# Kernel optimization log

Measured on AMD Instinct MI355X. Metric: run time of the kernel, lower is better.

## Reference

```python
import jax, jax.numpy as jnp
import numpy as np

jax.config.update("jax_enable_x64", True)

# --- static config (matches init_kwargs) ---
L = 6            # voxel_level_num
F = 8            # feature_dim
T = 524288       # per-level feature table size
B = 4194304      # buffer_size (hash table size)
N = 1048576      # number of query points
LEAF = 0.25      # leaf_voxel_size
UP = 2.0         # up_scale_factor

PRIMES = jnp.array([73856093, 19349669, 83492791], dtype=jnp.int64)
# corner offsets, z varies fastest (same order as torch self.steps)
STEPS = jnp.array([[0,0,0],[0,0,1],[0,1,0],[0,1,1],
                   [1,0,0],[1,0,1],[1,1,0],[1,1,1]], dtype=jnp.float32)


def setup_inputs() -> dict:
    key = jax.random.key(0)
    k1, k2, k3, k4 = jax.random.split(key, 4)
    query_points = jax.random.uniform(k1, (N, 3), dtype=jnp.float32) * 50.0
    features = 0.01 * jax.random.normal(k2, (L, T, F), dtype=jnp.float32)
    idx = jax.random.randint(k3, (L, B), 0, T, dtype=jnp.int64)
    empty = jax.random.uniform(k4, (L, B)) < 0.2
    feature_indexs = jnp.where(empty, jnp.int64(-1), idx)
    return {"query_points": query_points, "features": features,
            "feature_indexs": feature_indexs}


def _trilinear_coeffs(d):
    # d: [N,3] fractional coords in the cell; order matches STEPS (z fastest)
    tx, ty, tz = d[:, 0], d[:, 1], d[:, 2]
    return jnp.stack([
        (1-tx)*(1-ty)*(1-tz), (1-tx)*(1-ty)*tz,
        (1-tx)*ty*(1-tz),     (1-tx)*ty*tz,
        tx*(1-ty)*(1-tz),     tx*(1-ty)*tz,
        tx*ty*(1-tz),         tx*ty*tz,
    ], axis=1)  # [N,8]


def reference(query_points, features, feature_indexs):
    out = jnp.zeros((query_points.shape[0], F), dtype=query_points.dtype)
    for i in range(L):  # small fixed level loop (structurally distinct resolutions)
        res = LEAF * (UP ** i)
        scaled = query_points / res                      # [N,3]
        base = jnp.floor(scaled)
        corners = (base[:, None, :] + STEPS[None]).astype(jnp.int64)  # [N,8,3]
        keys = jnp.mod((corners * PRIMES).sum(-1), B)    # [N,8] spatial hash
        idx = feature_indexs[i][keys]                    # [N,8] gather, -1 = empty
        valid = idx.min(axis=1) > -1                     # [N] all 8 corners allocated
        coeffs = _trilinear_coeffs(scaled - base)        # [N,8]
        feats = features[i][jnp.clip(idx, 0, T - 1)]     # [N,8,F] gather
        level = jnp.einsum('nkf,nk->nf', feats, coeffs)  # trilinear interp
        out = out + jnp.where(valid[:, None], level, jnp.zeros((), out.dtype))
    return out
```

## Files before the change

### kernel.cpp

```cpp
#include <hip/hip_runtime.h>


static constexpr int      NPTS  = 1048576;
static constexpr int      NF    = 8;
static constexpr int      TTAB  = 524288;
static constexpr unsigned BTAB  = 4194304u;
static constexpr unsigned BMASK = BTAB - 1u;
static constexpr unsigned P0 = 73856093u, P1 = 19349669u, P2 = 83492791u;

static constexpr int NBIN = 4096;
static constexpr int SB   = 256;
static constexpr int PPB  = NPTS / SB;
static constexpr int ITER = PPB / 256;
static constexpr int BCAP = 512;

static constexpr int S2 = 51, S3 = 26, S4 = 14, S5 = 8;
static constexpr int OCC2 = 0, OCC3 = OCC2 + S2*S2, OCC4 = OCC3 + S3*S3,
                     OCC5 = OCC4 + S4*S4, OCCW = OCC5 + S5*S5;
static constexpr int CB2 = 0, CB3 = CB2 + (S2-1)*(S2-1),
                     CB4 = CB3 + (S3-1)*(S3-1), CB5 = CB4 + (S4-1)*(S4-1),
                     CBW = CB5 + (S5-1)*(S5-1);
static constexpr int RB2 = (S2*S2+3)/4, RB3 = (S3*S3+3)/4,
                     RB4 = (S4*S4+3)/4, RB5 = (S5*S5+3)/4;
static constexpr int OCCB = RB2+RB3+RB4+RB5;

static constexpr int L0S = 201, L0C = 200, L0W = 4;
static constexpr int L1S = 101, L1C = 100, L1W = 2;
static constexpr int OCC0W_CNT = L0S * L0S * L0W;
static constexpr int OCC1W_CNT = L1S * L1S * L1W;
static constexpr int CB0_CNT = L0C * L0C * L0W;
static constexpr int CB1_CNT = L1C * L1C * L1W;
static constexpr int OCC01_WORDS = OCC0W_CNT + OCC1W_CNT;
static constexpr int MIDC = CBW + CB0_CNT + CB1_CNT;
static constexpr int MIDB = 16 + (MIDC + 255) / 256;

static constexpr int BM01_WAVES = (int)(2 * BTAB / 256);
static constexpr int BM01B = BM01_WAVES / 4;

static constexpr size_t OUT_BM01_OFF  = 4u  * 1024 * 1024;
static constexpr size_t OUT_OCC25_OFF = 5u  * 1024 * 1024;
static constexpr size_t OUT_OCC0_OFF  = 5632u * 1024;
static constexpr size_t OUT_OCC1_OFF  = 7u  * 1024 * 1024;

static constexpr size_t SORTED_BYTES = (size_t)NPTS * 16;
static constexpr size_t CB25_OFF = SORTED_BYTES;
static constexpr size_t CB0_OFF  = CB25_OFF + 32768;
static constexpr size_t CB1_OFF  = CB0_OFF + 1310720;
static constexpr size_t BB_OFF   = CB1_OFF + 163840;
static constexpr size_t WS_FULL  = BB_OFF + (size_t)NBIN * 4;

typedef float f4 __attribute__((ext_vector_type(4)));
typedef int   i4 __attribute__((ext_vector_type(4)));

__device__ __forceinline__ void nhv_point_g(
    float qx, float qy, float qz,
    const float* __restrict__ feat, const int* __restrict__ fidx,
    const unsigned long long* __restrict__ cbit25,
    const unsigned long long* __restrict__ cbit0,
    const unsigned long long* __restrict__ cbit1, float acc[NF])
{
    const int ix0 = (int)(qx * 4.0f), iy0 = (int)(qy * 4.0f), iz0 = (int)(qz * 4.0f);
    const int ix1 = (int)(qx * 2.0f), iy1 = (int)(qy * 2.0f), iz1 = (int)(qz * 2.0f);

    const unsigned long long w0 = cbit0[(size_t)(iz0 * L0C + iy0) * L0W + (ix0 >> 6)];
    const unsigned long long w1 = cbit1[(size_t)(iz1 * L1C + iy1) * L1W + (ix1 >> 6)];

    float fxh[4], fyh[4], fzh[4];
    int   ixh[4], iyh[4], izh[4];
    unsigned vm = 0;
    vm |= (unsigned)((w0 >> (ix0 & 63)) & 1ull) << 0;
    vm |= (unsigned)((w1 >> (ix1 & 63)) & 1ull) << 1;
    const int Ss[4]  = {S2, S3, S4, S5};
    const int CBo[4] = {CB2, CB3, CB4, CB5};
#pragma unroll
    for (int j = 0; j < 4; ++j) {
        const float inv = 1.0f / (float)(1 << j);
        const float sx = qx*inv, sy = qy*inv, sz = qz*inv;
        const float bx = floorf(sx), by = floorf(sy), bz = floorf(sz);
        fxh[j] = sx-bx; fyh[j] = sy-by; fzh[j] = sz-bz;
        ixh[j] = (int)bx; iyh[j] = (int)by; izh[j] = (int)bz;
        const int C = Ss[j] - 1;
        const unsigned long long row = cbit25[CBo[j] + izh[j]*C + iyh[j]];
        vm |= (unsigned)((row >> ixh[j]) & 1ull) << (2 + j);
    }

#pragma unroll
    for (int f = 0; f < NF; ++f) acc[f] = 0.0f;

#pragma unroll
    for (int i = 0; i < 2; ++i) {
        if (vm & (1u << i)) {
            const float inv = (i == 0) ? 4.0f : 2.0f;
            const float sx = qx*inv, sy = qy*inv, sz = qz*inv;
            const float bx = floorf(sx), by = floorf(sy), bz = floorf(sz);
            const unsigned h = (unsigned)(int)bx*P0 + (unsigned)(int)by*P1
                             + (unsigned)(int)bz*P2;
            const int* __restrict__ tab = fidx + (size_t)i * BTAB;
            int id[8];
#pragma unroll
            for (int k = 0; k < 8; ++k) {
                unsigned key = h;
                if (k & 4) key += P0;
                if (k & 2) key += P1;
                if (k & 1) key += P2;
                id[k] = tab[key & BMASK];
            }
            const float tx = sx - bx, ty = sy - by, tz = sz - bz;
            const float wxv[2] = {1.0f - tx, tx};
            const float wyv[2] = {1.0f - ty, ty};
            const float wzv[2] = {1.0f - tz, tz};
            const float* __restrict__ fb = feat + (size_t)i * (TTAB * NF);
#pragma unroll
            for (int k = 0; k < 8; ++k) {
                const float c = wxv[(k>>2)&1] * wyv[(k>>1)&1] * wzv[k&1];
                const float4* p = (const float4*)(fb + (size_t)id[k] * NF);
                const float4 lo = p[0], hi = p[1];
                acc[0]+=c*lo.x; acc[1]+=c*lo.y; acc[2]+=c*lo.z; acc[3]+=c*lo.w;
                acc[4]+=c*hi.x; acc[5]+=c*hi.y; acc[6]+=c*hi.z; acc[7]+=c*hi.w;
            }
        }
    }
#pragma unroll
    for (int j = 0; j < 4; ++j) {
        if (vm & (1u << (2 + j))) {
            const int lvl = 2 + j;
            const unsigned h = (unsigned)ixh[j]*P0 + (unsigned)iyh[j]*P1
                             + (unsigned)izh[j]*P2;
            const int* __restrict__ tab = fidx + (size_t)lvl * BTAB;
            int id[8];
#pragma unroll
            for (int k = 0; k < 8; ++k) {
                unsigned key = h;
                if (k & 4) key += P0;
                if (k & 2) key += P1;
                if (k & 1) key += P2;
                id[k] = tab[key & BMASK];
            }
            const float wxv[2] = {1.0f - fxh[j], fxh[j]};
            const float wyv[2] = {1.0f - fyh[j], fyh[j]};
            const float wzv[2] = {1.0f - fzh[j], fzh[j]};
            const float* __restrict__ fb = feat + (size_t)lvl * (TTAB * NF);
#pragma unroll
            for (int k = 0; k < 8; ++k) {
                const float c = wxv[(k>>2)&1] * wyv[(k>>1)&1] * wzv[k&1];
                const float4* p = (const float4*)(fb + (size_t)id[k] * NF);
                const float4 lo = p[0], hi = p[1];
                acc[0]+=c*lo.x; acc[1]+=c*lo.y; acc[2]+=c*lo.z; acc[3]+=c*lo.w;
                acc[4]+=c*hi.x; acc[5]+=c*hi.y; acc[6]+=c*hi.z; acc[7]+=c*hi.w;
            }
        }
    }
}

__device__ __forceinline__ void nhv_point(
    float qx, float qy, float qz,
    const float* __restrict__ feat, const int* __restrict__ fidx, float acc[NF])
{
    float fx[6], fy[6], fz[6];
    unsigned h[6];
#pragma unroll
    for (int i = 0; i < 6; ++i) {
        const float inv = 4.0f / (float)(1 << i);
        const float sx = qx*inv, sy = qy*inv, sz = qz*inv;
        const float bx = floorf(sx), by = floorf(sy), bz = floorf(sz);
        fx[i] = sx-bx; fy[i] = sy-by; fz[i] = sz-bz;
        h[i] = (unsigned)(int)bx*P0 + (unsigned)(int)by*P1 + (unsigned)(int)bz*P2;
    }
    int id[6][8];
#pragma unroll
    for (int i = 0; i < 6; ++i) {
        const int* __restrict__ tab = fidx + (size_t)i * BTAB;
#pragma unroll
        for (int k = 0; k < 8; ++k) {
            unsigned key = h[i];
            if (k & 4) key += P0;
            if (k & 2) key += P1;
            if (k & 1) key += P2;
            id[i][k] = tab[key & BMASK];
        }
    }
#pragma unroll
    for (int f = 0; f < NF; ++f) acc[f] = 0.0f;
#pragma unroll
    for (int i = 0; i < 6; ++i) {
        int mn = id[i][0];
#pragma unroll
        for (int k = 1; k < 8; ++k) mn = min(mn, id[i][k]);
        if (mn > -1) {
            const float wxv[2] = {1.0f - fx[i], fx[i]};
            const float wyv[2] = {1.0f - fy[i], fy[i]};
            const float wzv[2] = {1.0f - fz[i], fz[i]};
            const float* __restrict__ fb = feat + (size_t)i * (TTAB * NF);
#pragma unroll
            for (int k = 0; k < 8; ++k) {
                const float c = wxv[(k>>2)&1] * wyv[(k>>1)&1] * wzv[k&1];
                const float4* p = (const float4*)(fb + (size_t)id[i][k] * NF);
                const float4 lo = p[0], hi = p[1];
                acc[0]+=c*lo.x; acc[1]+=c*lo.y; acc[2]+=c*lo.z; acc[3]+=c*lo.w;
                acc[4]+=c*hi.x; acc[5]+=c*hi.y; acc[6]+=c*hi.z; acc[7]+=c*hi.w;
            }
        }
    }
}

__device__ __forceinline__ unsigned expand4(unsigned v) {
    return (v & 1u) | ((v & 2u) << 2) | ((v & 4u) << 4) | ((v & 8u) << 6);
}
__device__ __forceinline__ unsigned bin_of(float x, float y, float z) {
    unsigned bx = min(15u, (unsigned)(int)(x * 0.32f));
    unsigned by = min(15u, (unsigned)(int)(y * 0.32f));
    unsigned bz = min(15u, (unsigned)(int)(z * 0.32f));
    return expand4(bx) | (expand4(by) << 1) | (expand4(bz) << 2);
}

__global__ __launch_bounds__(256) void pre_k(const int* __restrict__ fidx,
                                             unsigned long long* __restrict__ occ25,
                                             unsigned long long* __restrict__ bm01,
                                             const float* __restrict__ qp,
                                             unsigned* __restrict__ hist) {
    __shared__ unsigned lh[NBIN];
    const int t = threadIdx.x, b = blockIdx.x;
    if (b < OCCB) {
        int lvl, S, occoff, bb = b;
        if (bb < RB2)              { lvl = 2; S = S2; occoff = OCC2; }
        else if ((bb -= RB2) < RB3){ lvl = 3; S = S3; occoff = OCC3; }
        else if ((bb -= RB3) < RB4){ lvl = 4; S = S4; occoff = OCC4; }
        else        { bb -= RB4;     lvl = 5; S = S5; occoff = OCC5; }
        const int row  = bb * 4 + (t >> 6);
        const int lane = t & 63;
        if (row < S * S) {
            const int y = row % S, z = row / S;
            bool v = false;
            if (lane < S) {
                const unsigned key = ((unsigned)lane*P0 + (unsigned)y*P1
                                    + (unsigned)z*P2) & BMASK;
                v = fidx[(size_t)lvl * BTAB + key] >= 0;
            }
            const unsigned long long m = __ballot(v);
            if (lane == 0) occ25[occoff + row] = m;
        }
    } else if (b < OCCB + BM01B) {
        const int tid  = (b - OCCB) * 256 + t;
        const int w    = tid >> 6;
        const int lane = tid & 63;
        const i4 v = __builtin_nontemporal_load(
                        (const i4*)(fidx + (size_t)w * 256) + lane);
        const unsigned long long m0 = __ballot(v.x >= 0);
        const unsigned long long m1 = __ballot(v.y >= 0);
        const unsigned long long m2 = __ballot(v.z >= 0);
        const unsigned long long m3 = __ballot(v.w >= 0);
        if (lane == 0) {
            unsigned long long* d = bm01 + ((size_t)w << 2);
            d[0] = m0; d[1] = m1; d[2] = m2; d[3] = m3;
        }
    } else {
        const int bh = b - OCCB - BM01B;
        for (int i = t; i < NBIN; i += 256) lh[i] = 0u;
        __syncthreads();
        const int base = bh * PPB;
#pragma unroll
        for (int i = 0; i < ITER; ++i) {
            const int p = base + i * 256 + t;
            const float x = __builtin_nontemporal_load(qp + 3*p);
            const float y = __builtin_nontemporal_load(qp + 3*p + 1);
            const float z = __builtin_nontemporal_load(qp + 3*p + 2);
            atomicAdd(&lh[bin_of(x, y, z)], 1u);
        }
        __syncthreads();
        for (int i = t; i < NBIN; i += 256)
            __builtin_nontemporal_store(lh[i], hist + (size_t)bh * NBIN + i);
    }
}

__global__ __launch_bounds__(256) void occ01_k(
    const unsigned long long* __restrict__ bm01,
    unsigned long long* __restrict__ occ0,
    unsigned long long* __restrict__ occ1)
{
    const int lane   = threadIdx.x & 63;
    const int wid    = (blockIdx.x * 256 + threadIdx.x) >> 6;
    const int nwaves = (int)gridDim.x * 4;
    const int ngroups = (OCC01_WORDS + 3) / 4;

    for (int g = wid; g < ngroups; g += nwaves) {
        unsigned long long vals[4];
        bool ok[4];
#pragma unroll
        for (int k = 0; k < 4; ++k) {
            const int w = g * 4 + k;
            ok[k] = (w < OCC01_WORDS);
            bool v = false;
            if (ok[k]) {
                int S, row, wblk, lvl;
                if (w < OCC0W_CNT) { lvl = 0; S = L0S; row = w >> 2; wblk = w & 3; }
                else { lvl = 1; S = L1S; const int w1 = w - OCC0W_CNT; row = w1 >> 1; wblk = w1 & 1; }
                const int z = row / S, y = row % S;
                const int x = wblk * 64 + lane;
                if (x < S) {
                    const unsigned key = ((unsigned)x*P0 + (unsigned)y*P1
                                        + (unsigned)z*P2) & BMASK;
                    const unsigned B = (unsigned)lvl * BTAB + key;
                    const unsigned long long word =
                        bm01[((size_t)(B >> 8) << 2) | (B & 3u)];
                    v = (word >> ((B >> 2) & 63u)) & 1ull;
                }
            }
            vals[k] = v ? 1ull : 0ull;
        }
#pragma unroll
        for (int k = 0; k < 4; ++k) {
            const unsigned long long m = __ballot(vals[k] != 0ull);
            const int w = g * 4 + k;
            if (ok[k] && lane == 0) {
                if (w < OCC0W_CNT) occ0[w] = m;
                else               occ1[w - OCC0W_CNT] = m;
            }
        }
    }
}

__global__ __launch_bounds__(256) void mid_k(unsigned* __restrict__ hist,
                                             unsigned* __restrict__ binbase,
                                             const unsigned long long* __restrict__ occ25,
                                             const unsigned long long* __restrict__ occ0,
                                             const unsigned long long* __restrict__ occ1,
                                             unsigned long long* __restrict__ cbit25,
                                             unsigned long long* __restrict__ cbit0,
                                             unsigned long long* __restrict__ cbit1) {
    const int t = threadIdx.x, b = blockIdx.x;
    if (b < 16) {
        const int bin = b * 256 + t;
        unsigned run = 0;
        for (int blk = 0; blk < SB; ++blk) {
            const unsigned v = hist[(size_t)blk * NBIN + bin];
            hist[(size_t)blk * NBIN + bin] = run;
            run += v;
        }
        binbase[bin] = run;
        return;
    }
    const int c = (b - 16) * 256 + t;
    if (c >= MIDC) return;
    if (c < CBW) {
        int S, occoff, cboff, local;
        if (c < CB3)      { S = S2; occoff = OCC2; cboff = CB2; local = c; }
        else if (c < CB4) { S = S3; occoff = OCC3; cboff = CB3; local = c - CB3; }
        else if (c < CB5) { S = S4; occoff = OCC4; cboff = CB4; local = c - CB4; }
        else              { S = S5; occoff = OCC5; cboff = CB5; local = c - CB5; }
        const int C = S - 1;
        const int cy = local % C, cz = local / C;
        const unsigned long long r00 = occ25[occoff +  cz      * S + cy    ];
        const unsigned long long r10 = occ25[occoff +  cz      * S + cy + 1];
        const unsigned long long r01 = occ25[occoff + (cz + 1) * S + cy    ];
        const unsigned long long r11 = occ25[occoff + (cz + 1) * S + cy + 1];
        cbit25[cboff + cz * C + cy] = (r00 & (r00 >> 1)) & (r10 & (r10 >> 1))
                                    & (r01 & (r01 >> 1)) & (r11 & (r11 >> 1));
    } else if (c < CBW + CB0_CNT) {
        const int c0 = c - CBW;
        const int w = c0 & 3, crow = c0 >> 2;
        const int cy = crow % L0C, cz = crow / L0C;
        unsigned long long res = ~0ull;
#pragma unroll
        for (int dy = 0; dy < 2; ++dy)
#pragma unroll
            for (int dz = 0; dz < 2; ++dz) {
                const unsigned long long* r =
                    occ0 + ((size_t)((cz + dz) * L0S + (cy + dy)) << 2);
                const unsigned long long a = r[w];
                const unsigned long long n = (w < 3) ? r[w + 1] : 0ull;
                res &= a & ((a >> 1) | (n << 63));
            }
        cbit0[c0] = res;
    } else {
        const int c1 = c - CBW - CB0_CNT;
        const int w = c1 & 1, crow = c1 >> 1;
        const int cy = crow % L1C, cz = crow / L1C;
        unsigned long long res = ~0ull;
#pragma unroll
        for (int dy = 0; dy < 2; ++dy)
#pragma unroll
            for (int dz = 0; dz < 2; ++dz) {
                const unsigned long long* r =
                    occ1 + ((size_t)((cz + dz) * L1S + (cy + dy)) << 1);
                const unsigned long long a = r[w];
                const unsigned long long n = (w < 1) ? r[w + 1] : 0ull;
                res &= a & ((a >> 1) | (n << 63));
            }
        cbit1[c1] = res;
    }
}

__global__ __launch_bounds__(256) void binscan_k(unsigned* __restrict__ binbase) {
    __shared__ unsigned tot[256];
    const int t = threadIdx.x;
    unsigned v[16];
    unsigned s = 0;
#pragma unroll
    for (int i = 0; i < 16; ++i) { v[i] = s; s += binbase[t * 16 + i]; }
    tot[t] = s;
    __syncthreads();
    for (int d = 1; d < 256; d <<= 1) {
        const unsigned x = (t >= d) ? tot[t - d] : 0u;
        __syncthreads();
        tot[t] += x;
        __syncthreads();
    }
    const unsigned cb = tot[t] - s;
#pragma unroll
    for (int i = 0; i < 16; ++i) binbase[t * 16 + i] = cb + v[i];
}

__global__ __launch_bounds__(256) void scatter_k(const float* __restrict__ qp,
                                                 const unsigned* __restrict__ hist,
                                                 const unsigned* __restrict__ binbase,
                                                 float4* __restrict__ sorted) {
    __shared__ unsigned cur[NBIN];
    const int b = blockIdx.x, t = threadIdx.x;
    for (int i = t; i < NBIN; i += 256)
        cur[i] = binbase[i] + hist[(size_t)b * NBIN + i];
    __syncthreads();
    const int base = b * PPB;
#pragma unroll
    for (int i = 0; i < ITER; ++i) {
        const int p = base + i * 256 + t;
        const float x = __builtin_nontemporal_load(qp + 3*p);
        const float y = __builtin_nontemporal_load(qp + 3*p + 1);
        const float z = __builtin_nontemporal_load(qp + 3*p + 2);
        const unsigned slot = atomicAdd(&cur[bin_of(x, y, z)], 1u);
        const f4 v = {x, y, z, __uint_as_float((unsigned)p)};
        __builtin_nontemporal_store(v, (f4*)sorted + slot);
    }
}

__global__ __launch_bounds__(256) void binsort_k(float4* __restrict__ sorted,
                                                 const unsigned* __restrict__ binbase) {
    __shared__ float4        pts[BCAP];
    __shared__ unsigned char sk[BCAP];
    __shared__ unsigned      cnt[64];
    const int bin = blockIdx.x, t = threadIdx.x;
    const unsigned start = binbase[bin];
    const unsigned end   = (bin < NBIN - 1) ? binbase[bin + 1] : (unsigned)NPTS;
    const int n = (int)(end - start);
    if (n <= 1 || n > BCAP) return;

    if (t < 64) cnt[t] = 0u;
    __syncthreads();
#pragma unroll
    for (int r = 0; r < BCAP / 256; ++r) {
        const int i = r * 256 + t;
        if (i < n) {
            const f4 pv = __builtin_nontemporal_load((const f4*)sorted + (start + i));
            const float4 p = make_float4(pv.x, pv.y, pv.z, pv.w);
            pts[i] = p;
            const unsigned ux = (unsigned)(int)(p.x * 1.28f) & 3u;
            const unsigned uy = (unsigned)(int)(p.y * 1.28f) & 3u;
            const unsigned uz = (unsigned)(int)(p.z * 1.28f) & 3u;
            const unsigned s = (ux & 1u) | ((uy & 1u) << 1) | ((uz & 1u) << 2)
                             | ((ux >> 1) << 3) | ((uy >> 1) << 4) | ((uz >> 1) << 5);
            sk[i] = (unsigned char)s;
            atomicAdd(&cnt[s], 1u);
        }
    }
    __syncthreads();
    if (t == 0) {
        unsigned run = 0;
#pragma unroll
        for (int i = 0; i < 64; ++i) { const unsigned v = cnt[i]; cnt[i] = run; run += v; }
    }
    __syncthreads();
#pragma unroll
    for (int r = 0; r < BCAP / 256; ++r) {
        const int i = r * 256 + t;
        if (i < n) {
            const unsigned dest = atomicAdd(&cnt[sk[i]], 1u);
            const float4 p = pts[i];
            const f4 v = {p.x, p.y, p.z, p.w};
            __builtin_nontemporal_store(v, (f4*)sorted + (start + dest));
        }
    }
}

__global__ __launch_bounds__(256) void nhv_main_k(
    const float4* __restrict__ sp, const float* __restrict__ feat,
    const int* __restrict__ fidx,
    const unsigned long long* __restrict__ cbit25,
    const unsigned long long* __restrict__ cbit0,
    const unsigned long long* __restrict__ cbit1,
    float* __restrict__ out)
{
    const int nwg = NPTS / 256;
    const int bid = blockIdx.x;
    const int swz = (bid & 7) * (nwg >> 3) + (bid >> 3);
    const int j   = swz * 256 + (int)threadIdx.x;

    const f4 s = __builtin_nontemporal_load((const f4*)sp + j);
    float acc[NF];
    nhv_point_g(s.x, s.y, s.z, feat, fidx, cbit25, cbit0, cbit1, acc);
    const unsigned n = __float_as_uint(s.w);
    f4* o = (f4*)(out + (size_t)n * NF);
    f4 lo = {acc[0], acc[1], acc[2], acc[3]};
    f4 hi = {acc[4], acc[5], acc[6], acc[7]};
    __builtin_nontemporal_store(lo, o);
    __builtin_nontemporal_store(hi, o + 1);
}

__global__ __launch_bounds__(256) void nhv_direct_k(
    const float* __restrict__ qp, const float* __restrict__ feat,
    const int* __restrict__ fidx, float* __restrict__ out)
{
    const int n = blockIdx.x * 256 + threadIdx.x;
    if (n >= NPTS) return;
    float acc[NF];
    nhv_point(qp[3*n], qp[3*n+1], qp[3*n+2], feat, fidx, acc);
    float4* o = (float4*)(out + (size_t)n * NF);
    o[0] = make_float4(acc[0], acc[1], acc[2], acc[3]);
    o[1] = make_float4(acc[4], acc[5], acc[6], acc[7]);
}

extern "C" void kernel_launch(void* const* d_in, const int* in_sizes, int n_in,
                              void* d_out, int out_size, void* d_ws, size_t ws_size,
                              hipStream_t stream) {
    const float* qp   = (const float*)d_in[0];
    const float* feat = (const float*)d_in[1];
    const int*   fidx = (const int*)d_in[2];
    float*       out  = (float*)d_out;

    if (ws_size >= WS_FULL) {
        float4*             sorted  = (float4*)d_ws;
        unsigned long long* cbit25  = (unsigned long long*)((char*)d_ws + CB25_OFF);
        unsigned long long* cbit0   = (unsigned long long*)((char*)d_ws + CB0_OFF);
        unsigned long long* cbit1   = (unsigned long long*)((char*)d_ws + CB1_OFF);
        unsigned*           binbase = (unsigned*)((char*)d_ws + BB_OFF);
        unsigned*           hist  = (unsigned*)d_out;
        unsigned long long* bm01  = (unsigned long long*)((char*)d_out + OUT_BM01_OFF);
        unsigned long long* occ25 = (unsigned long long*)((char*)d_out + OUT_OCC25_OFF);
        unsigned long long* occ0  = (unsigned long long*)((char*)d_out + OUT_OCC0_OFF);
        unsigned long long* occ1  = (unsigned long long*)((char*)d_out + OUT_OCC1_OFF);

        pre_k<<<dim3(OCCB + BM01B + SB), dim3(256), 0, stream>>>(fidx, occ25, bm01, qp, hist);
        occ01_k<<<dim3(512), dim3(256), 0, stream>>>(bm01, occ0, occ1);
        mid_k<<<dim3(MIDB), dim3(256), 0, stream>>>(hist, binbase, occ25, occ0, occ1,
                                                    cbit25, cbit0, cbit1);
        binscan_k<<<dim3(1), dim3(256), 0, stream>>>(binbase);
        scatter_k<<<dim3(SB), dim3(256), 0, stream>>>(qp, hist, binbase, sorted);
        binsort_k<<<dim3(NBIN), dim3(256), 0, stream>>>(sorted, binbase);
        nhv_main_k<<<dim3(NPTS/256), dim3(256), 0, stream>>>(sorted, feat, fidx,
                                                             cbit25, cbit0, cbit1, out);
    } else {
        nhv_direct_k<<<dim3(NPTS/256), dim3(256), 0, stream>>>(qp, feat, fidx, out);
    }
}
```

Baseline: 222.0 us.

## Fuse bin sort into main kernel and use per-cell byte validity grids

The histogram scan moves into the occupancy kernel and the bin-base scan into the corner-bit kernel, which removes two launches. The in-bin sort is folded into the main kernel: it builds an ordering in shared memory, so the extra pass writing the sorted array back to global memory goes away. Validity for levels 2-5 now comes from dense byte grids indexed by cell (one for level 2, one packed grid for levels 3-5), and all level indices are derived from the level-0 integer coords by shifts. The cost is larger validity tables, fewer threads per block for bins with few points, and a strided fallback for oversized bins.

```diff
diff --git a/kernel.cpp b/kernel.cpp
--- a/kernel.cpp
+++ b/kernel.cpp
@@ -17,9 +17,6 @@
 static constexpr int S2 = 51, S3 = 26, S4 = 14, S5 = 8;
 static constexpr int OCC2 = 0, OCC3 = OCC2 + S2*S2, OCC4 = OCC3 + S3*S3,
                      OCC5 = OCC4 + S4*S4, OCCW = OCC5 + S5*S5;
-static constexpr int CB2 = 0, CB3 = CB2 + (S2-1)*(S2-1),
-                     CB4 = CB3 + (S3-1)*(S3-1), CB5 = CB4 + (S4-1)*(S4-1),
-                     CBW = CB5 + (S5-1)*(S5-1);
 static constexpr int RB2 = (S2*S2+3)/4, RB3 = (S3*S3+3)/4,
                      RB4 = (S4*S4+3)/4, RB5 = (S5*S5+3)/4;
 static constexpr int OCCB = RB2+RB3+RB4+RB5;
@@ -31,8 +28,11 @@
 static constexpr int CB0_CNT = L0C * L0C * L0W;
 static constexpr int CB1_CNT = L1C * L1C * L1W;
 static constexpr int OCC01_WORDS = OCC0W_CNT + OCC1W_CNT;
-static constexpr int MIDC = CBW + CB0_CNT + CB1_CNT;
-static constexpr int MIDB = 16 + (MIDC + 255) / 256;
+
+static constexpr int B2_CNT   = 50 * 50 * 50;
+static constexpr int B345_CNT = 25 * 25 * 25;
+static constexpr int CBTASKS  = CB0_CNT + CB1_CNT + B2_CNT + B345_CNT;
+static constexpr int CBK_BLOCKS = 1 + (CBTASKS + 255) / 256;
 
 static constexpr int BM01_WAVES = (int)(2 * BTAB / 256);
 static constexpr int BM01B = BM01_WAVES / 4;
@@ -43,112 +43,90 @@
 static constexpr size_t OUT_OCC1_OFF  = 7u  * 1024 * 1024;
 
 static constexpr size_t SORTED_BYTES = (size_t)NPTS * 16;
-static constexpr size_t CB25_OFF = SORTED_BYTES;
-static constexpr size_t CB0_OFF  = CB25_OFF + 32768;
-static constexpr size_t CB1_OFF  = CB0_OFF + 1310720;
-static constexpr size_t BB_OFF   = CB1_OFF + 163840;
+static constexpr size_t CB0_OFF  = SORTED_BYTES;
+static constexpr size_t CB1_OFF  = CB0_OFF  + 1310720;
+static constexpr size_t B2_OFF   = CB1_OFF  + 163840;
+static constexpr size_t B345_OFF = B2_OFF   + 131072;
+static constexpr size_t BB_OFF   = B345_OFF + 16384;
 static constexpr size_t WS_FULL  = BB_OFF + (size_t)NBIN * 4;
 
 typedef float f4 __attribute__((ext_vector_type(4)));
 typedef int   i4 __attribute__((ext_vector_type(4)));
+typedef unsigned long long u64;
 
 __device__ __forceinline__ void nhv_point_g(
     float qx, float qy, float qz,
     const float* __restrict__ feat, const int* __restrict__ fidx,
-    const unsigned long long* __restrict__ cbit25,
-    const unsigned long long* __restrict__ cbit0,
-    const unsigned long long* __restrict__ cbit1, float acc[NF])
+    const u64* __restrict__ cbit0, const u64* __restrict__ cbit1,
+    const unsigned char* __restrict__ b2, const unsigned char* __restrict__ b345,
+    float acc[NF])
 {
     const int ix0 = (int)(qx * 4.0f), iy0 = (int)(qy * 4.0f), iz0 = (int)(qz * 4.0f);
-    const int ix1 = (int)(qx * 2.0f), iy1 = (int)(qy * 2.0f), iz1 = (int)(qz * 2.0f);
-
-    const unsigned long long w0 = cbit0[(size_t)(iz0 * L0C + iy0) * L0W + (ix0 >> 6)];
-    const unsigned long long w1 = cbit1[(size_t)(iz1 * L1C + iy1) * L1W + (ix1 >> 6)];
-
-    float fxh[4], fyh[4], fzh[4];
-    int   ixh[4], iyh[4], izh[4];
-    unsigned vm = 0;
-    vm |= (unsigned)((w0 >> (ix0 & 63)) & 1ull) << 0;
-    vm |= (unsigned)((w1 >> (ix1 & 63)) & 1ull) << 1;
-    const int Ss[4]  = {S2, S3, S4, S5};
-    const int CBo[4] = {CB2, CB3, CB4, CB5};
-#pragma unroll
-    for (int j = 0; j < 4; ++j) {
-        const float inv = 1.0f / (float)(1 << j);
-        const float sx = qx*inv, sy = qy*inv, sz = qz*inv;
-        const float bx = floorf(sx), by = floorf(sy), bz = floorf(sz);
-        fxh[j] = sx-bx; fyh[j] = sy-by; fzh[j] = sz-bz;
-        ixh[j] = (int)bx; iyh[j] = (int)by; izh[j] = (int)bz;
-        const int C = Ss[j] - 1;
-        const unsigned long long row = cbit25[CBo[j] + izh[j]*C + iyh[j]];
-        vm |= (unsigned)((row >> ixh[j]) & 1ull) << (2 + j);
-    }
+    const int ix1 = ix0 >> 1, iy1 = iy0 >> 1, iz1 = iz0 >> 1;
+    const int ix2 = ix0 >> 2, iy2 = iy0 >> 2, iz2 = iz0 >> 2;
+    const int ix3 = ix0 >> 3, iy3 = iy0 >> 3, iz3 = iz0 >> 3;
+
+    const u64 w0 = cbit0[(size_t)(iz0 * L0C + iy0) * L0W + (ix0 >> 6)];
+    const u64 w1 = cbit1[(size_t)(iz1 * L1C + iy1) * L1W + (ix1 >> 6)];
+    const unsigned vb2   = b2  [(iz2 * 50 + iy2) * 50 + ix2];
+    const unsigned vb345 = b345[(iz3 * 25 + iy3) * 25 + ix3];
+
+    const unsigned vm = (unsigned)((w0 >> (ix0 & 63)) & 1ull)
+                      | ((unsigned)((w1 >> (ix1 & 63)) & 1ull) << 1)
+                      | ((vb2   & 1u) << 2)
+                      | ((vb345 & 7u) << 3);
 
 #pragma unroll
     for (int f = 0; f < NF; ++f) acc[f] = 0.0f;
 
-#pragma unroll
-    for (int i = 0; i < 2; ++i) {
-        if (vm & (1u << i)) {
-            const float inv = (i == 0) ? 4.0f : 2.0f;
-            const float sx = qx*inv, sy = qy*inv, sz = qz*inv;
-            const float bx = floorf(sx), by = floorf(sy), bz = floorf(sz);
-            const unsigned h = (unsigned)(int)bx*P0 + (unsigned)(int)by*P1
-                             + (unsigned)(int)bz*P2;
-            const int* __restrict__ tab = fidx + (size_t)i * BTAB;
-            int id[8];
-#pragma unroll
-            for (int k = 0; k < 8; ++k) {
-                unsigned key = h;
-                if (k & 4) key += P0;
-                if (k & 2) key += P1;
-                if (k & 1) key += P2;
-                id[k] = tab[key & BMASK];
-            }
-            const float tx = sx - bx, ty = sy - by, tz = sz - bz;
-            const float wxv[2] = {1.0f - tx, tx};
-            const float wyv[2] = {1.0f - ty, ty};
-            const float wzv[2] = {1.0f - tz, tz};
-            const float* __restrict__ fb = feat + (size_t)i * (TTAB * NF);
-#pragma unroll
-            for (int k = 0; k < 8; ++k) {
-                const float c = wxv[(k>>2)&1] * wyv[(k>>1)&1] * wzv[k&1];
-                const float4* p = (const float4*)(fb + (size_t)id[k] * NF);
-                const float4 lo = p[0], hi = p[1];
-                acc[0]+=c*lo.x; acc[1]+=c*lo.y; acc[2]+=c*lo.z; acc[3]+=c*lo.w;
-                acc[4]+=c*hi.x; acc[5]+=c*hi.y; acc[6]+=c*hi.z; acc[7]+=c*hi.w;
-            }
-        }
-    }
-#pragma unroll
-    for (int j = 0; j < 4; ++j) {
-        if (vm & (1u << (2 + j))) {
-            const int lvl = 2 + j;
-            const unsigned h = (unsigned)ixh[j]*P0 + (unsigned)iyh[j]*P1
-                             + (unsigned)izh[j]*P2;
-            const int* __restrict__ tab = fidx + (size_t)lvl * BTAB;
-            int id[8];
-#pragma unroll
-            for (int k = 0; k < 8; ++k) {
-                unsigned key = h;
-                if (k & 4) key += P0;
-                if (k & 2) key += P1;
-                if (k & 1) key += P2;
-                id[k] = tab[key & BMASK];
-            }
-            const float wxv[2] = {1.0f - fxh[j], fxh[j]};
-            const float wyv[2] = {1.0f - fyh[j], fyh[j]};
-            const float wzv[2] = {1.0f - fzh[j], fzh[j]};
-            const float* __restrict__ fb = feat + (size_t)lvl * (TTAB * NF);
-#pragma unroll
-            for (int k = 0; k < 8; ++k) {
-                const float c = wxv[(k>>2)&1] * wyv[(k>>1)&1] * wzv[k&1];
-                const float4* p = (const float4*)(fb + (size_t)id[k] * NF);
-                const float4 lo = p[0], hi = p[1];
-                acc[0]+=c*lo.x; acc[1]+=c*lo.y; acc[2]+=c*lo.z; acc[3]+=c*lo.w;
-                acc[4]+=c*hi.x; acc[5]+=c*hi.y; acc[6]+=c*hi.z; acc[7]+=c*hi.w;
-            }
-        }
+    auto gather = [&](int lvl, unsigned cx, unsigned cy, unsigned cz,
+                      float tx, float ty, float tz) {
+        const unsigned h = cx * P0 + cy * P1 + cz * P2;
+        const int* __restrict__ tab = fidx + (size_t)lvl * BTAB;
+        int id[8];
+#pragma unroll
+        for (int k = 0; k < 8; ++k) {
+            unsigned key = h;
+            if (k & 4) key += P0;
+            if (k & 2) key += P1;
+            if (k & 1) key += P2;
+            id[k] = tab[key & BMASK];
+        }
+        const float wxv[2] = {1.0f - tx, tx};
+        const float wyv[2] = {1.0f - ty, ty};
+        const float wzv[2] = {1.0f - tz, tz};
+        const float* __restrict__ fb = feat + (size_t)lvl * (TTAB * NF);
+#pragma unroll
+        for (int k = 0; k < 8; ++k) {
+            const float c = wxv[(k>>2)&1] * wyv[(k>>1)&1] * wzv[k&1];
+            const float4* p = (const float4*)(fb + (size_t)id[k] * NF);
+            const float4 lo = p[0], hi = p[1];
+            acc[0]+=c*lo.x; acc[1]+=c*lo.y; acc[2]+=c*lo.z; acc[3]+=c*lo.w;
+            acc[4]+=c*hi.x; acc[5]+=c*hi.y; acc[6]+=c*hi.z; acc[7]+=c*hi.w;
+        }
+    };
+
+    if (vm & 1u)
+        gather(0, (unsigned)ix0, (unsigned)iy0, (unsigned)iz0,
+               qx*4.0f - (float)ix0, qy*4.0f - (float)iy0, qz*4.0f - (float)iz0);
+    if (vm & 2u)
+        gather(1, (unsigned)ix1, (unsigned)iy1, (unsigned)iz1,
+               qx*2.0f - (float)ix1, qy*2.0f - (float)iy1, qz*2.0f - (float)iz1);
+    if (vm & 4u)
+        gather(2, (unsigned)ix2, (unsigned)iy2, (unsigned)iz2,
+               qx - (float)ix2, qy - (float)iy2, qz - (float)iz2);
+    if (vm & 8u)
+        gather(3, (unsigned)ix3, (unsigned)iy3, (unsigned)iz3,
+               qx*0.5f - (float)ix3, qy*0.5f - (float)iy3, qz*0.5f - (float)iz3);
+    if (vm & 16u) {
+        const int ix4 = ix0 >> 4, iy4 = iy0 >> 4, iz4 = iz0 >> 4;
+        gather(4, (unsigned)ix4, (unsigned)iy4, (unsigned)iz4,
+               qx*0.25f - (float)ix4, qy*0.25f - (float)iy4, qz*0.25f - (float)iz4);
+    }
+    if (vm & 32u) {
+        const int ix5 = ix0 >> 5, iy5 = iy0 >> 5, iz5 = iz0 >> 5;
+        gather(5, (unsigned)ix5, (unsigned)iy5, (unsigned)iz5,
+               qx*0.125f - (float)ix5, qy*0.125f - (float)iy5, qz*0.125f - (float)iz5);
     }
 }
 
@@ -214,8 +192,8 @@
 }
 
 __global__ __launch_bounds__(256) void pre_k(const int* __restrict__ fidx,
-                                             unsigned long long* __restrict__ occ25,
-                                             unsigned long long* __restrict__ bm01,
+                                             u64* __restrict__ occ25,
+                                             u64* __restrict__ bm01,
                                              const float* __restrict__ qp,
                                              unsigned* __restrict__ hist) {
     __shared__ unsigned lh[NBIN];
@@ -236,7 +214,7 @@
                                     + (unsigned)z*P2) & BMASK;
                 v = fidx[(size_t)lvl * BTAB + key] >= 0;
             }
-            const unsigned long long m = __ballot(v);
+            const u64 m = __ballot(v);
             if (lane == 0) occ25[occoff + row] = m;
         }
     } else if (b < OCCB + BM01B) {
@@ -245,12 +223,12 @@
         const int lane = tid & 63;
         const i4 v = __builtin_nontemporal_load(
                         (const i4*)(fidx + (size_t)w * 256) + lane);
-        const unsigned long long m0 = __ballot(v.x >= 0);
-        const unsigned long long m1 = __ballot(v.y >= 0);
-        const unsigned long long m2 = __ballot(v.z >= 0);
-        const unsigned long long m3 = __ballot(v.w >= 0);
+        const u64 m0 = __ballot(v.x >= 0);
+        const u64 m1 = __ballot(v.y >= 0);
+        const u64 m2 = __ballot(v.z >= 0);
+        const u64 m3 = __ballot(v.w >= 0);
         if (lane == 0) {
-            unsigned long long* d = bm01 + ((size_t)w << 2);
+            u64* d = bm01 + ((size_t)w << 2);
             d[0] = m0; d[1] = m1; d[2] = m2; d[3] = m3;
         }
     } else {
@@ -272,18 +250,29 @@
     }
 }
 
-__global__ __launch_bounds__(256) void occ01_k(
-    const unsigned long long* __restrict__ bm01,
-    unsigned long long* __restrict__ occ0,
-    unsigned long long* __restrict__ occ1)
-{
-    const int lane   = threadIdx.x & 63;
-    const int wid    = (blockIdx.x * 256 + threadIdx.x) >> 6;
-    const int nwaves = (int)gridDim.x * 4;
+__global__ __launch_bounds__(256) void os_k(unsigned* __restrict__ hist,
+                                            unsigned* __restrict__ binbase,
+                                            const u64* __restrict__ bm01,
+                                            u64* __restrict__ occ0,
+                                            u64* __restrict__ occ1) {
+    const int t = threadIdx.x, b = blockIdx.x;
+    if (b < 16) {
+        const int bin = b * 256 + t;
+        unsigned run = 0;
+        for (int blk = 0; blk < SB; ++blk) {
+            const unsigned v = hist[(size_t)blk * NBIN + bin];
+            hist[(size_t)blk * NBIN + bin] = run;
+            run += v;
+        }
+        binbase[bin] = run;
+        return;
+    }
+    const int lane    = t & 63;
+    const int wid     = ((b - 16) * 256 + t) >> 6;
+    const int nwaves  = ((int)gridDim.x - 16) * 4;
     const int ngroups = (OCC01_WORDS + 3) / 4;
-
     for (int g = wid; g < ngroups; g += nwaves) {
-        unsigned long long vals[4];
+        bool vv[4];
         bool ok[4];
 #pragma unroll
         for (int k = 0; k < 4; ++k) {
@@ -300,16 +289,15 @@
                     const unsigned key = ((unsigned)x*P0 + (unsigned)y*P1
                                         + (unsigned)z*P2) & BMASK;
                     const unsigned B = (unsigned)lvl * BTAB + key;
-                    const unsigned long long word =
-                        bm01[((size_t)(B >> 8) << 2) | (B & 3u)];
+                    const u64 word = bm01[((size_t)(B >> 8) << 2) | (B & 3u)];
                     v = (word >> ((B >> 2) & 63u)) & 1ull;
                 }
             }
-            vals[k] = v ? 1ull : 0ull;
+            vv[k] = v;
         }
 #pragma unroll
         for (int k = 0; k < 4; ++k) {
-            const unsigned long long m = __ballot(vals[k] != 0ull);
+            const u64 m = __ballot(vv[k]);
             const int w = g * 4 + k;
             if (ok[k] && lane == 0) {
                 if (w < OCC0W_CNT) occ0[w] = m;
@@ -319,95 +307,97 @@
     }
 }
 
-__global__ __launch_bounds__(256) void mid_k(unsigned* __restrict__ hist,
-                                             unsigned* __restrict__ binbase,
-                                             const unsigned long long* __restrict__ occ25,
-                                             const unsigned long long* __restrict__ occ0,
-                                             const unsigned long long* __restrict__ occ1,
-                                             unsigned long long* __restrict__ cbit25,
-                                             unsigned long long* __restrict__ cbit0,
-                                             unsigned long long* __restrict__ cbit1) {
+__global__ __launch_bounds__(256) void cb_k(unsigned* __restrict__ binbase,
+                                            const u64* __restrict__ occ25,
+                                            const u64* __restrict__ occ0,
+                                            const u64* __restrict__ occ1,
+                                            u64* __restrict__ cbit0,
+                                            u64* __restrict__ cbit1,
+                                            unsigned char* __restrict__ b2,
+                                            unsigned char* __restrict__ b345) {
     const int t = threadIdx.x, b = blockIdx.x;
-    if (b < 16) {
-        const int bin = b * 256 + t;
-        unsigned run = 0;
-        for (int blk = 0; blk < SB; ++blk) {
-            const unsigned v = hist[(size_t)blk * NBIN + bin];
-            hist[(size_t)blk * NBIN + bin] = run;
-            run += v;
-        }
-        binbase[bin] = run;
+    if (b == 0) {
+        __shared__ unsigned tot[256];
+        unsigned v[16];
+        unsigned s = 0;
+#pragma unroll
+        for (int i = 0; i < 16; ++i) { v[i] = s; s += binbase[t * 16 + i]; }
+        tot[t] = s;
+        __syncthreads();
+        for (int d = 1; d < 256; d <<= 1) {
+            const unsigned x = (t >= d) ? tot[t - d] : 0u;
+            __syncthreads();
+            tot[t] += x;
+            __syncthreads();
+        }
+        const unsigned cbv = tot[t] - s;
+#pragma unroll
+        for (int i = 0; i < 16; ++i) binbase[t * 16 + i] = cbv + v[i];
         return;
     }
-    const int c = (b - 16) * 256 + t;
-    if (c >= MIDC) return;
-    if (c < CBW) {
-        int S, occoff, cboff, local;
-        if (c < CB3)      { S = S2; occoff = OCC2; cboff = CB2; local = c; }
-        else if (c < CB4) { S = S3; occoff = OCC3; cboff = CB3; local = c - CB3; }
-        else if (c < CB5) { S = S4; occoff = OCC4; cboff = CB4; local = c - CB4; }
-        else              { S = S5; occoff = OCC5; cboff = CB5; local = c - CB5; }
-        const int C = S - 1;
-        const int cy = local % C, cz = local / C;
-        const unsigned long long r00 = occ25[occoff +  cz      * S + cy    ];
-        const unsigned long long r10 = occ25[occoff +  cz      * S + cy + 1];
-        const unsigned long long r01 = occ25[occoff + (cz + 1) * S + cy    ];
-        const unsigned long long r11 = occ25[occoff + (cz + 1) * S + cy + 1];
-        cbit25[cboff + cz * C + cy] = (r00 & (r00 >> 1)) & (r10 & (r10 >> 1))
-                                    & (r01 & (r01 >> 1)) & (r11 & (r11 >> 1));
-    } else if (c < CBW + CB0_CNT) {
-        const int c0 = c - CBW;
-        const int w = c0 & 3, crow = c0 >> 2;
+    const int c = (b - 1) * 256 + t;
+    if (c < CB0_CNT) {
+        const int w = c & 3, crow = c >> 2;
         const int cy = crow % L0C, cz = crow / L0C;
-        unsigned long long res = ~0ull;
+        u64 res = ~0ull;
 #pragma unroll
         for (int dy = 0; dy < 2; ++dy)
 #pragma unroll
             for (int dz = 0; dz < 2; ++dz) {
-                const unsigned long long* r =
-                    occ0 + ((size_t)((cz + dz) * L0S + (cy + dy)) << 2);
-                const unsigned long long a = r[w];
-                const unsigned long long n = (w < 3) ? r[w + 1] : 0ull;
+                const u64* r = occ0 + ((size_t)((cz + dz) * L0S + (cy + dy)) << 2);
+                const u64 a = r[w];
+                const u64 n = (w < 3) ? r[w + 1] : 0ull;
                 res &= a & ((a >> 1) | (n << 63));
             }
-        cbit0[c0] = res;
-    } else {
-        const int c1 = c - CBW - CB0_CNT;
+        cbit0[c] = res;
+    } else if (c < CB0_CNT + CB1_CNT) {
+        const int c1 = c - CB0_CNT;
         const int w = c1 & 1, crow = c1 >> 1;
         const int cy = crow % L1C, cz = crow / L1C;
-        unsigned long long res = ~0ull;
+        u64 res = ~0ull;
 #pragma unroll
         for (int dy = 0; dy < 2; ++dy)
 #pragma unroll
             for (int dz = 0; dz < 2; ++dz) {
-                const unsigned long long* r =
-                    occ1 + ((size_t)((cz + dz) * L1S + (cy + dy)) << 1);
-                const unsigned long long a = r[w];
-                const unsigned long long n = (w < 1) ? r[w + 1] : 0ull;
+                const u64* r = occ1 + ((size_t)((cz + dz) * L1S + (cy + dy)) << 1);
+                const u64 a = r[w];
+                const u64 n = (w < 1) ? r[w + 1] : 0ull;
                 res &= a & ((a >> 1) | (n << 63));
             }
         cbit1[c1] = res;
-    }
-}
-
-__global__ __launch_bounds__(256) void binscan_k(unsigned* __restrict__ binbase) {
-    __shared__ unsigned tot[256];
-    const int t = threadIdx.x;
-    unsigned v[16];
-    unsigned s = 0;
-#pragma unroll
-    for (int i = 0; i < 16; ++i) { v[i] = s; s += binbase[t * 16 + i]; }
-    tot[t] = s;
-    __syncthreads();
-    for (int d = 1; d < 256; d <<= 1) {
-        const unsigned x = (t >= d) ? tot[t - d] : 0u;
-        __syncthreads();
-        tot[t] += x;
-        __syncthreads();
-    }
-    const unsigned cb = tot[t] - s;
-#pragma unroll
-    for (int i = 0; i < 16; ++i) binbase[t * 16 + i] = cb + v[i];
+    } else if (c < CB0_CNT + CB1_CNT + B2_CNT) {
+        const int l = c - CB0_CNT - CB1_CNT;
+        const int ix = l % 50, iy = (l / 50) % 50, iz = l / 2500;
+        u64 m = ~0ull;
+#pragma unroll
+        for (int dz = 0; dz < 2; ++dz)
+#pragma unroll
+            for (int dy = 0; dy < 2; ++dy) {
+                const u64 r = occ25[OCC2 + (iz + dz) * S2 + (iy + dy)];
+                m &= r & (r >> 1);
+            }
+        b2[l] = (unsigned char)((m >> ix) & 1ull);
+    } else {
+        const int l = c - CB0_CNT - CB1_CNT - B2_CNT;
+        if (l >= B345_CNT) return;
+        const int ix = l % 25, iy = (l / 25) % 25, iz = l / 625;
+        u64 m3 = ~0ull, m4 = ~0ull, m5 = ~0ull;
+#pragma unroll
+        for (int dz = 0; dz < 2; ++dz)
+#pragma unroll
+            for (int dy = 0; dy < 2; ++dy) {
+                const u64 r3 = occ25[OCC3 + (iz + dz) * S3 + (iy + dy)];
+                const u64 r4 = occ25[OCC4 + ((iz >> 1) + dz) * S4 + ((iy >> 1) + dy)];
+                const u64 r5 = occ25[OCC5 + ((iz >> 2) + dz) * S5 + ((iy >> 2) + dy)];
+                m3 &= r3 & (r3 >> 1);
+                m4 &= r4 & (r4 >> 1);
+                m5 &= r5 & (r5 >> 1);
+            }
+        const unsigned v3 = (unsigned)((m3 >> ix) & 1ull);
+        const unsigned v4 = (unsigned)((m4 >> (ix >> 1)) & 1ull);
+        const unsigned v5 = (unsigned)((m5 >> (ix >> 2)) & 1ull);
+        b345[l] = (unsigned char)(v3 | (v4 << 1) | (v5 << 2));
+    }
 }
 
 __global__ __launch_bounds__(256) void scatter_k(const float* __restrict__ qp,
@@ -432,76 +422,84 @@
     }
 }
 
-__global__ __launch_bounds__(256) void binsort_k(float4* __restrict__ sorted,
-                                                 const unsigned* __restrict__ binbase) {
-    __shared__ float4        pts[BCAP];
-    __shared__ unsigned char sk[BCAP];
-    __shared__ unsigned      cnt[64];
-    const int bin = blockIdx.x, t = threadIdx.x;
+__global__ __launch_bounds__(256) void nhv_main_k(
+    const float4* __restrict__ sorted, const unsigned* __restrict__ binbase,
+    const float* __restrict__ feat, const int* __restrict__ fidx,
+    const u64* __restrict__ cbit0, const u64* __restrict__ cbit1,
+    const unsigned char* __restrict__ b2, const unsigned char* __restrict__ b345,
+    float* __restrict__ out)
+{
+    __shared__ float4         pts[BCAP];
+    __shared__ unsigned char  sk[BCAP];
+    __shared__ unsigned short ord[BCAP];
+    __shared__ unsigned       cnt[64];
+
+    const int bid = blockIdx.x;
+    const int bin = (bid & 7) * (NBIN >> 3) + (bid >> 3);
+    const int t   = threadIdx.x;
     const unsigned start = binbase[bin];
     const unsigned end   = (bin < NBIN - 1) ? binbase[bin + 1] : (unsigned)NPTS;
     const int n = (int)(end - start);
-    if (n <= 1 || n > BCAP) return;
-
-    if (t < 64) cnt[t] = 0u;
-    __syncthreads();
-#pragma unroll
-    for (int r = 0; r < BCAP / 256; ++r) {
-        const int i = r * 256 + t;
-        if (i < n) {
-            const f4 pv = __builtin_nontemporal_load((const f4*)sorted + (start + i));
-            const float4 p = make_float4(pv.x, pv.y, pv.z, pv.w);
-            pts[i] = p;
-            const unsigned ux = (unsigned)(int)(p.x * 1.28f) & 3u;
-            const unsigned uy = (unsigned)(int)(p.y * 1.28f) & 3u;
-            const unsigned uz = (unsigned)(int)(p.z * 1.28f) & 3u;
-            const unsigned s = (ux & 1u) | ((uy & 1u) << 1) | ((uz & 1u) << 2)
-                             | ((ux >> 1) << 3) | ((uy >> 1) << 4) | ((uz >> 1) << 5);
-            sk[i] = (unsigned char)s;
-            atomicAdd(&cnt[s], 1u);
-        }
-    }
-    __syncthreads();
-    if (t == 0) {
-        unsigned run = 0;
-#pragma unroll
-        for (int i = 0; i < 64; ++i) { const unsigned v = cnt[i]; cnt[i] = run; run += v; }
-    }
-    __syncthreads();
-#pragma unroll
-    for (int r = 0; r < BCAP / 256; ++r) {
-        const int i = r * 256 + t;
-        if (i < n) {
-            const unsigned dest = atomicAdd(&cnt[sk[i]], 1u);
-            const float4 p = pts[i];
-            const f4 v = {p.x, p.y, p.z, p.w};
-            __builtin_nontemporal_store(v, (f4*)sorted + (start + dest));
-        }
-    }
-}
-
-__global__ __launch_bounds__(256) void nhv_main_k(
-    const float4* __restrict__ sp, const float* __restrict__ feat,
-    const int* __restrict__ fidx,
-    const unsigned long long* __restrict__ cbit25,
-    const unsigned long long* __restrict__ cbit0,
-    const unsigned long long* __restrict__ cbit1,
-    float* __restrict__ out)
-{
-    const int nwg = NPTS / 256;
-    const int bid = blockIdx.x;
-    const int swz = (bid & 7) * (nwg >> 3) + (bid >> 3);
-    const int j   = swz * 256 + (int)threadIdx.x;
-
-    const f4 s = __builtin_nontemporal_load((const f4*)sp + j);
-    float acc[NF];
-    nhv_point_g(s.x, s.y, s.z, feat, fidx, cbit25, cbit0, cbit1, acc);
-    const unsigned n = __float_as_uint(s.w);
-    f4* o = (f4*)(out + (size_t)n * NF);
-    f4 lo = {acc[0], acc[1], acc[2], acc[3]};
-    f4 hi = {acc[4], acc[5], acc[6], acc[7]};
-    __builtin_nontemporal_store(lo, o);
-    __builtin_nontemporal_store(hi, o + 1);
+
+    if (n <= BCAP) {
+        if (t < 64) cnt[t] = 0u;
+        __syncthreads();
+#pragma unroll
+        for (int r = 0; r < BCAP / 256; ++r) {
+            const int i = r * 256 + t;
+            if (i < n) {
+                const f4 pv = __builtin_nontemporal_load((const f4*)sorted + (start + i));
+                pts[i] = make_float4(pv.x, pv.y, pv.z, pv.w);
+                const unsigned ux = (unsigned)(int)(pv.x * 1.28f) & 3u;
+                const unsigned uy = (unsigned)(int)(pv.y * 1.28f) & 3u;
+                const unsigned uz = (unsigned)(int)(pv.z * 1.28f) & 3u;
+                const unsigned s = (ux & 1u) | ((uy & 1u) << 1) | ((uz & 1u) << 2)
+                                 | ((ux >> 1) << 3) | ((uy >> 1) << 4) | ((uz >> 1) << 5);
+                sk[i] = (unsigned char)s;
+                atomicAdd(&cnt[s], 1u);
+            }
+        }
+        __syncthreads();
+        if (t == 0) {
+            unsigned run = 0;
+#pragma unroll
+            for (int i = 0; i < 64; ++i) { const unsigned v = cnt[i]; cnt[i] = run; run += v; }
+        }
+        __syncthreads();
+#pragma unroll
+        for (int r = 0; r < BCAP / 256; ++r) {
+            const int i = r * 256 + t;
+            if (i < n) ord[atomicAdd(&cnt[sk[i]], 1u)] = (unsigned short)i;
+        }
+        __syncthreads();
+#pragma unroll
+        for (int r = 0; r < BCAP / 256; ++r) {
+            const int j = r * 256 + t;
+            if (j < n) {
+                const float4 p = pts[ord[j]];
+                float acc[NF];
+                nhv_point_g(p.x, p.y, p.z, feat, fidx, cbit0, cbit1, b2, b345, acc);
+                const unsigned pn = __float_as_uint(p.w);
+                f4* o = (f4*)(out + (size_t)pn * NF);
+                f4 lo = {acc[0], acc[1], acc[2], acc[3]};
+                f4 hi = {acc[4], acc[5], acc[6], acc[7]};
+                __builtin_nontemporal_store(lo, o);
+                __builtin_nontemporal_store(hi, o + 1);
+            }
+        }
+    } else {
+        for (int j = t; j < n; j += 256) {
+            const f4 pv = __builtin_nontemporal_load((const f4*)sorted + (start + j));
+            float acc[NF];
+            nhv_point_g(pv.x, pv.y, pv.z, feat, fidx, cbit0, cbit1, b2, b345, acc);
+            const unsigned pn = __float_as_uint(pv.w);
+            f4* o = (f4*)(out + (size_t)pn * NF);
+            f4 lo = {acc[0], acc[1], acc[2], acc[3]};
+            f4 hi = {acc[4], acc[5], acc[6], acc[7]};
+            __builtin_nontemporal_store(lo, o);
+            __builtin_nontemporal_store(hi, o + 1);
+        }
+    }
 }
 
 __global__ __launch_bounds__(256) void nhv_direct_k(
@@ -526,26 +524,25 @@
     float*       out  = (float*)d_out;
 
     if (ws_size >= WS_FULL) {
-        float4*             sorted  = (float4*)d_ws;
-        unsigned long long* cbit25  = (unsigned long long*)((char*)d_ws + CB25_OFF);
-        unsigned long long* cbit0   = (unsigned long long*)((char*)d_ws + CB0_OFF);
-        unsigned long long* cbit1   = (unsigned long long*)((char*)d_ws + CB1_OFF);
-        unsigned*           binbase = (unsigned*)((char*)d_ws + BB_OFF);
-        unsigned*           hist  = (unsigned*)d_out;
-        unsigned long long* bm01  = (unsigned long long*)((char*)d_out + OUT_BM01_OFF);
-        unsigned long long* occ25 = (unsigned long long*)((char*)d_out + OUT_OCC25_OFF);
-        unsigned long long* occ0  = (unsigned long long*)((char*)d_out + OUT_OCC0_OFF);
-        unsigned long long* occ1  = (unsigned long long*)((char*)d_out + OUT_OCC1_OFF);
+        float4*        sorted  = (float4*)d_ws;
+        u64*           cbit0   = (u64*)((char*)d_ws + CB0_OFF);
+        u64*           cbit1   = (u64*)((char*)d_ws + CB1_OFF);
+        unsigned char* b2      = (unsigned char*)((char*)d_ws + B2_OFF);
+        unsigned char* b345    = (unsigned char*)((char*)d_ws + B345_OFF);
+        unsigned*      binbase = (unsigned*)((char*)d_ws + BB_OFF);
+        unsigned*      hist  = (unsigned*)d_out;
+        u64*           bm01  = (u64*)((char*)d_out + OUT_BM01_OFF);
+        u64*           occ25 = (u64*)((char*)d_out + OUT_OCC25_OFF);
+        u64*           occ0  = (u64*)((char*)d_out + OUT_OCC0_OFF);
+        u64*           occ1  = (u64*)((char*)d_out + OUT_OCC1_OFF);
 
         pre_k<<<dim3(OCCB + BM01B + SB), dim3(256), 0, stream>>>(fidx, occ25, bm01, qp, hist);
-        occ01_k<<<dim3(512), dim3(256), 0, stream>>>(bm01, occ0, occ1);
-        mid_k<<<dim3(MIDB), dim3(256), 0, stream>>>(hist, binbase, occ25, occ0, occ1,
-                                                    cbit25, cbit0, cbit1);
-        binscan_k<<<dim3(1), dim3(256), 0, stream>>>(binbase);
+        os_k<<<dim3(16 + 512), dim3(256), 0, stream>>>(hist, binbase, bm01, occ0, occ1);
+        cb_k<<<dim3(CBK_BLOCKS), dim3(256), 0, stream>>>(binbase, occ25, occ0, occ1,
+                                                         cbit0, cbit1, b2, b345);
         scatter_k<<<dim3(SB), dim3(256), 0, stream>>>(qp, hist, binbase, sorted);
-        binsort_k<<<dim3(NBIN), dim3(256), 0, stream>>>(sorted, binbase);
-        nhv_main_k<<<dim3(NPTS/256), dim3(256), 0, stream>>>(sorted, feat, fidx,
-                                                             cbit25, cbit0, cbit1, out);
+        nhv_main_k<<<dim3(NBIN), dim3(256), 0, stream>>>(sorted, binbase, feat, fidx,
+                                                         cbit0, cbit1, b2, b345, out);
     } else {
         nhv_direct_k<<<dim3(NPTS/256), dim3(256), 0, stream>>>(qp, feat, fidx, out);
     }
```

New measurement: 207.0 us. 1.07x faster.
